# Performance work log

Hardware: AMD Instinct MI355X
Metric: run time of the kernel (lower is better)

The kernel has to match this reference:

```python
import jax, jax.numpy as jnp
import numpy as np

N = 50000
H = 8
D = 32
E = 400000
IN = 128
NEG_SLOPE = 0.2


def _gat(h, edges, W, al, ar, b):
    # DGL GATConv: fc -> per-head attention logits -> edge softmax over dst -> aggregate
    src, dst = edges[0], edges[1]
    feat = (h @ W).reshape(N, H, D)                      # [N,H,D]
    el = jnp.einsum('nhd,hd->nh', feat, al)              # [N,H]
    er = jnp.einsum('nhd,hd->nh', feat, ar)              # [N,H]
    e = jax.nn.leaky_relu(el[src] + er[dst], NEG_SLOPE)  # [E,H]
    m = jax.ops.segment_max(e, dst, num_segments=N)      # [N,H] per-dst max
    m = jnp.where(jnp.isfinite(m), m, 0.0)
    m = jax.lax.stop_gradient(m)
    ex = jnp.exp(e - m[dst])                             # [E,H]
    denom = jax.ops.segment_sum(ex, dst, num_segments=N) # [N,H]
    alpha = ex / denom[dst]                              # edge softmax
    out = jax.ops.segment_sum(feat[src] * alpha[:, :, None], dst, num_segments=N)  # [N,H,D]
    return (out + b.reshape(1, H, D)).reshape(N, H * D)


def setup_inputs() -> dict:
    key = jax.random.key(0)
    ks = jax.random.split(key, 12)
    s = 0.05
    return {
        'h': jax.random.normal(ks[0], (N, IN), jnp.float32),
        'edges0': jax.random.randint(ks[1], (2, E), 0, N, jnp.int32),
        'edges1': jax.random.randint(ks[2], (2, E), 0, N, jnp.int32),
        'fc0': jax.random.normal(ks[3], (IN, H * D), jnp.float32) * s,
        'al0': jax.random.normal(ks[4], (H, D), jnp.float32) * s,
        'ar0': jax.random.normal(ks[5], (H, D), jnp.float32) * s,
        'bias0': jnp.zeros((H * D,), jnp.float32),
        'fc1': jax.random.normal(ks[6], (IN, H * D), jnp.float32) * s,
        'al1': jax.random.normal(ks[7], (H, D), jnp.float32) * s,
        'ar1': jax.random.normal(ks[8], (H, D), jnp.float32) * s,
        'bias1': jnp.zeros((H * D,), jnp.float32),
        'sw1': jax.random.normal(ks[9], (H * D, 128), jnp.float32) * s,
        'sb1': jnp.zeros((128,), jnp.float32),
        'sw2': jax.random.normal(ks[10], (128, 1), jnp.float32) * s,
    }


def reference(h, edges0, edges1, fc0, al0, ar0, bias0, fc1, al1, ar1, bias1, sw1, sb1, sw2):
    z0 = _gat(h, edges0, fc0, al0, ar0, bias0)   # [N, H*D]
    z1 = _gat(h, edges1, fc1, al1, ar1, bias1)   # [N, H*D]
    z = jnp.stack([z0, z1], axis=1)              # [N, M=2, H*D]
    # semantic attention: MLP -> mean over nodes -> softmax over meta-paths
    w = jnp.tanh(z @ sw1 + sb1) @ sw2            # [N,M,1]
    beta = jax.nn.softmax(w.mean(axis=0), axis=0)  # [M,1]
    return (beta[None] * z).sum(axis=1)          # [N, H*D]
```

## Files before the change

kernel.cpp:

```cpp
#include <hip/hip_runtime.h>
#include <math.h>

#define NEG_SLOPE 0.2f

typedef unsigned int uint;
typedef unsigned short ushort;
typedef __bf16 bf16x8 __attribute__((ext_vector_type(8)));
typedef float f32x4 __attribute__((ext_vector_type(4)));

__device__ __forceinline__ uint bf16r(float a) {
    uint u = __float_as_uint(a);
    return (u + 0x7fffu + ((u >> 16) & 1u)) >> 16;
}
__device__ __forceinline__ uint bf16pack(float a, float b) {
    return bf16r(a) | (bf16r(b) << 16);
}
__device__ __forceinline__ float bflo(uint u) { return __uint_as_float(u << 16); }
__device__ __forceinline__ float bfhi(uint u) { return __uint_as_float(u & 0xffff0000u); }

__device__ __forceinline__ float fast_tanh(float x) {
    x = fminf(fmaxf(x, -15.f), 15.f);
    float t = __expf(2.f * x);
    return 1.f - 2.f * __builtin_amdgcn_rcpf(t + 1.f);
}

__global__ void prep_kernel(const float* __restrict__ fc0, const float* __restrict__ fc1,
                            const float* __restrict__ sw1, ushort* __restrict__ wbt,
                            ushort* __restrict__ sw1t, float* __restrict__ wsum,
                            int* __restrict__ count, int* __restrict__ cursor, int Ntot) {
    int b = blockIdx.x;
    if (b == 0 && threadIdx.x == 0) { wsum[0] = 0.f; wsum[1] = 0.f; }
    if (b < 256) {
        int idx = b * 256 + threadIdx.x;
        const float* W = (idx >> 15) ? fc1 : fc0;
        int r = idx & 32767;
        int c = r >> 7, k = r & 127;
        wbt[idx] = (ushort)bf16r(W[(size_t)k * 256 + c]);
    } else if (b < 384) {
        int idx = (b - 256) * 256 + threadIdx.x;
        int c = idx >> 8, p = idx & 255;
        int col = (p & ~63) + ((p & 3) * 16) + ((p >> 2) & 15);
        sw1t[idx] = (ushort)bf16r(sw1[(size_t)col * 128 + c]);
    } else {
        int i = (b - 384) * 256 + threadIdx.x;
        if (i < Ntot) { count[i] = 0; cursor[i] = 0; }
    }
}

__global__ void hist_kernel(const int* __restrict__ e0, const int* __restrict__ e1,
                            int* __restrict__ count, int E, int N) {
    int e = blockIdx.x * blockDim.x + threadIdx.x;
    if (e >= 2 * E) return;
    int l = (e >= E);
    int ee = e - l * E;
    const int* edges = l ? e1 : e0;
    atomicAdd(&count[edges[E + ee] + l * N], 1);
}

__global__ void scan1_kernel(const int* __restrict__ count, int* __restrict__ base,
                             int* __restrict__ bsum, int Ntot) {
    __shared__ int ws_s[4];
    int b = blockIdx.x;
    int i = b * 256 + threadIdx.x;
    int v = (i < Ntot) ? count[i] : 0;
    int lane = threadIdx.x & 63;
    int wid = threadIdx.x >> 6;
    int x = v;
#pragma unroll
    for (int s = 1; s < 64; s <<= 1) {
        int y = __shfl_up(x, s, 64);
        if (lane >= s) x += y;
    }
    if (lane == 63) ws_s[wid] = x;
    __syncthreads();
    int add = 0;
    for (int w = 0; w < wid; w++) add += ws_s[w];
    int incl = x + add;
    if (i < Ntot) base[i] = incl - v;
    if (threadIdx.x == 255) bsum[b] = incl;
}

__global__ void scan2_kernel(int* __restrict__ bsum, int nb) {
    __shared__ int ws_s[4];
    __shared__ int running_s;
    if (threadIdx.x == 0) running_s = 0;
    __syncthreads();
    int lane = threadIdx.x & 63;
    int wid = threadIdx.x >> 6;
    for (int c0 = 0; c0 < nb; c0 += 256) {
        int i = c0 + threadIdx.x;
        int v = (i < nb) ? bsum[i] : 0;
        int x = v;
#pragma unroll
        for (int s = 1; s < 64; s <<= 1) {
            int y = __shfl_up(x, s, 64);
            if (lane >= s) x += y;
        }
        if (lane == 63) ws_s[wid] = x;
        __syncthreads();
        int add = 0;
        for (int w = 0; w < wid; w++) add += ws_s[w];
        int incl = x + add;
        int run = running_s;
        if (i < nb) bsum[i] = run + incl - v;
        __syncthreads();
        if (threadIdx.x == 255) running_s = run + incl;
        __syncthreads();
    }
}

#define HKPAD 136
__global__ void __launch_bounds__(256, 4)
fc_kernel(const float* __restrict__ h, const ushort* __restrict__ wbt,
          const float* __restrict__ al0, const float* __restrict__ ar0,
          const float* __restrict__ al1, const float* __restrict__ ar1,
          ushort* __restrict__ featb, float* __restrict__ el,
          float* __restrict__ er, int N, int nb) {
    __shared__ ushort hs[64 * HKPAD];
    int b = blockIdx.x;
    int l = (b >= nb);
    int n0 = (b - l * nb) * 64;
    for (int t = threadIdx.x; t < 64 * 32; t += 256) {
        int r = t >> 5, i4 = t & 31;
        int n = n0 + r;
        float4 v = make_float4(0.f, 0.f, 0.f, 0.f);
        if (n < N) v = ((const float4*)h)[(size_t)n * 32 + i4];
        uint2 pk;
        pk.x = bf16pack(v.x, v.y);
        pk.y = bf16pack(v.z, v.w);
        *((uint2*)(hs + r * HKPAD + i4 * 4)) = pk;
    }
    __syncthreads();

    const ushort* wb = wbt + l * 32768;
    const float* al = l ? al1 : al0;
    const float* ar = l ? ar1 : ar0;
    ushort* fb = featb + (size_t)l * N * 256;
    float* elp = el + (size_t)l * N * 8;
    float* erp = er + (size_t)l * N * 8;

    int wv = threadIdx.x >> 6;
    int lane = threadIdx.x & 63;
    int lhi = lane >> 4, llo = lane & 15;

    f32x4 acc[4][4];
#pragma unroll
    for (int cb = 0; cb < 4; cb++)
#pragma unroll
        for (int rt = 0; rt < 4; rt++) acc[cb][rt] = (f32x4){0.f, 0.f, 0.f, 0.f};

#pragma unroll
    for (int ks = 0; ks < 4; ks++) {
        bf16x8 a[4];
#pragma unroll
        for (int rt = 0; rt < 4; rt++)
            a[rt] = *(const bf16x8*)(hs + (rt * 16 + llo) * HKPAD + ks * 32 + lhi * 8);
#pragma unroll
        for (int cb = 0; cb < 4; cb++) {
            bf16x8 bfrag = *(const bf16x8*)(wb + (size_t)(64 * wv + 16 * cb + llo) * 128 + ks * 32 + lhi * 8);
#pragma unroll
            for (int rt = 0; rt < 4; rt++)
                acc[cb][rt] = __builtin_amdgcn_mfma_f32_16x16x32_bf16(a[rt], bfrag, acc[cb][rt], 0, 0, 0);
        }
    }

    float alv0 = al[64 * wv + llo],      alv1 = al[64 * wv + 16 + llo];
    float alv2 = al[64 * wv + 32 + llo], alv3 = al[64 * wv + 48 + llo];
    float arv0 = ar[64 * wv + llo],      arv1 = ar[64 * wv + 16 + llo];
    float arv2 = ar[64 * wv + 32 + llo], arv3 = ar[64 * wv + 48 + llo];

#pragma unroll
    for (int rt = 0; rt < 4; rt++) {
#pragma unroll
        for (int reg = 0; reg < 4; reg++) {
            int n = n0 + rt * 16 + lhi * 4 + reg;
            bool valid = (n < N);
            uint2 pv;
            pv.x = bf16pack(acc[0][rt][reg], acc[1][rt][reg]);
            pv.y = bf16pack(acc[2][rt][reg], acc[3][rt][reg]);
            if (valid) *((uint2*)(fb + (size_t)n * 256 + 64 * wv + 4 * llo)) = pv;
            float pl0 = acc[0][rt][reg] * alv0 + acc[1][rt][reg] * alv1;
            float pl1 = acc[2][rt][reg] * alv2 + acc[3][rt][reg] * alv3;
            float pr0 = acc[0][rt][reg] * arv0 + acc[1][rt][reg] * arv1;
            float pr1 = acc[2][rt][reg] * arv2 + acc[3][rt][reg] * arv3;
#pragma unroll
            for (int s = 1; s <= 8; s <<= 1) {
                pl0 += __shfl_xor(pl0, s, 64);
                pl1 += __shfl_xor(pl1, s, 64);
                pr0 += __shfl_xor(pr0, s, 64);
                pr1 += __shfl_xor(pr1, s, 64);
            }
            if (llo == 0 && valid) {
                *((float2*)(elp + (size_t)n * 8 + 2 * wv)) = make_float2(pl0, pl1);
                *((float2*)(erp + (size_t)n * 8 + 2 * wv)) = make_float2(pr0, pr1);
            }
        }
    }
}

__global__ void scatter_kernel(const int* __restrict__ e0, const int* __restrict__ e1,
                               const float* __restrict__ el, const float* __restrict__ er,
                               const int* __restrict__ base, const int* __restrict__ bsum,
                               int* __restrict__ cursor, int* __restrict__ csr_src,
                               float* __restrict__ pedge, int E, int N) {
    int e = blockIdx.x * blockDim.x + threadIdx.x;
    if (e >= 2 * E) return;
    int l = (e >= E);
    int ee = e - l * E;
    const int* edges = l ? e1 : e0;
    int src = edges[ee];
    int dst = edges[E + ee];
    int d = dst + l * N;
    int pos = base[d] + bsum[d >> 8] + atomicAdd(&cursor[d], 1);
    csr_src[pos] = src;
    size_t so = (size_t)(l * N + src) * 2;
    size_t dofs = (size_t)(l * N + dst) * 2;
    float4 l0 = ((const float4*)el)[so];
    float4 l1 = ((const float4*)el)[so + 1];
    float4 r0 = ((const float4*)er)[dofs];
    float4 r1 = ((const float4*)er)[dofs + 1];
    float v[8] = {l0.x + r0.x, l0.y + r0.y, l0.z + r0.z, l0.w + r0.w,
                  l1.x + r1.x, l1.y + r1.y, l1.z + r1.z, l1.w + r1.w};
#pragma unroll
    for (int k = 0; k < 8; k++) {
        float t = (v[k] > 0.f) ? v[k] : NEG_SLOPE * v[k];
        v[k] = __expf(t);
    }
    ((float4*)pedge)[pos * 2]     = make_float4(v[0], v[1], v[2], v[3]);
    ((float4*)pedge)[pos * 2 + 1] = make_float4(v[4], v[5], v[6], v[7]);
}

#define AGG_STEP(qq, uu)                                        \
    d0 += (qq).x; d1 += (qq).y;                                 \
    a.x += (qq).x * bflo((uu).x); a.y += (qq).x * bfhi((uu).x); \
    a.z += (qq).y * bflo((uu).y); a.w += (qq).y * bfhi((uu).y);

__global__ void aggregate_csr_kernel(const int* __restrict__ csr_src, const float* __restrict__ pedge,
                                     const int* __restrict__ base, const int* __restrict__ bsum,
                                     const int* __restrict__ count, const ushort* __restrict__ featb,
                                     const float* __restrict__ bias0, const float* __restrict__ bias1,
                                     ushort* __restrict__ z0b, ushort* __restrict__ z1b, int N) {
    int wid = threadIdx.x >> 6;
    int lane = threadIdx.x & 63;
    int d = blockIdx.x * 4 + wid;
    if (d >= 2 * N) return;
    int l = (d >= N);
    int dst = d - l * N;
    int row0 = base[d] + bsum[d >> 8];
    int deg = count[d];
    int w = lane >> 4, llo = lane & 15;
    const float2* pe = (const float2*)(pedge + (size_t)row0 * 8);
    const int* cs = csr_src + row0;
    const uint2* fb2 = (const uint2*)(featb + (size_t)l * N * 256);

    float d0 = 0.f, d1 = 0.f;
    float4 a = make_float4(0.f, 0.f, 0.f, 0.f);
    int t = 0;
    for (; t + 8 <= deg; t += 8) {
        int s[8];
#pragma unroll
        for (int j = 0; j < 8; j++) s[j] = cs[t + j];
        float2 q[8];
#pragma unroll
        for (int j = 0; j < 8; j++) q[j] = pe[(t + j) * 4 + w];
        uint2 u[8];
#pragma unroll
        for (int j = 0; j < 8; j++) u[j] = fb2[(size_t)s[j] * 64 + lane];
#pragma unroll
        for (int j = 0; j < 8; j++) { AGG_STEP(q[j], u[j]) }
    }
    for (; t + 4 <= deg; t += 4) {
        int s[4];
#pragma unroll
        for (int j = 0; j < 4; j++) s[j] = cs[t + j];
        float2 q[4];
#pragma unroll
        for (int j = 0; j < 4; j++) q[j] = pe[(t + j) * 4 + w];
        uint2 u[4];
#pragma unroll
        for (int j = 0; j < 4; j++) u[j] = fb2[(size_t)s[j] * 64 + lane];
#pragma unroll
        for (int j = 0; j < 4; j++) { AGG_STEP(q[j], u[j]) }
    }
    for (; t < deg; t++) {
        int s0 = cs[t];
        float2 q0 = pe[t * 4 + w];
        uint2 u0 = fb2[(size_t)s0 * 64 + lane];
        AGG_STEP(q0, u0)
    }
    const float* bias = l ? bias1 : bias0;
    int c0 = 64 * w + llo;
    float b0 = bias[c0], b1 = bias[c0 + 16], b2 = bias[c0 + 32], b3 = bias[c0 + 48];
    float i0 = (d0 > 0.f) ? 1.f / d0 : 0.f;
    float i1 = (d1 > 0.f) ? 1.f / d1 : 0.f;
    uint2 o;
    o.x = bf16pack(a.x * i0 + b0, a.y * i0 + b1);
    o.y = bf16pack(a.z * i1 + b2, a.w * i1 + b3);
    ushort* zb = l ? z1b : z0b;
    ((uint2*)zb)[(size_t)dst * 64 + lane] = o;
}

#define ZROW 264
__global__ void __launch_bounds__(256, 4)
semantic_kernel(const ushort* __restrict__ z0b, const ushort* __restrict__ z1b,
                const ushort* __restrict__ sw1t, const float* __restrict__ sb1,
                const float* __restrict__ sw2, float* __restrict__ wsum, int N) {
    __shared__ ushort zs[64 * ZROW];
    __shared__ float rowp[64];
    int n0 = blockIdx.x * 32;
    if (threadIdx.x < 64) rowp[threadIdx.x] = 0.f;
    for (int t = threadIdx.x; t < 64 * 32; t += 256) {
        int row = t >> 5, i16 = t & 31;
        int r = row >> 1, mm = row & 1;
        int n = n0 + r;
        uint4 v = make_uint4(0u, 0u, 0u, 0u);
        if (n < N) v = ((const uint4*)(mm ? z1b : z0b))[(size_t)n * 32 + i16];
        *((uint4*)(zs + row * ZROW + i16 * 8)) = v;
    }
    __syncthreads();

    int wv = threadIdx.x >> 6;
    int lane = threadIdx.x & 63;
    int lhi = lane >> 4, llo = lane & 15;

    f32x4 acc[2][4];
#pragma unroll
    for (int c = 0; c < 2; c++)
#pragma unroll
        for (int rt = 0; rt < 4; rt++) acc[c][rt] = (f32x4){0.f, 0.f, 0.f, 0.f};

#pragma unroll
    for (int ks = 0; ks < 8; ks++) {
        bf16x8 b0 = *(const bf16x8*)(sw1t + (size_t)((2 * wv) * 16 + llo) * 256 + ks * 32 + lhi * 8);
        bf16x8 b1 = *(const bf16x8*)(sw1t + (size_t)((2 * wv + 1) * 16 + llo) * 256 + ks * 32 + lhi * 8);
#pragma unroll
        for (int rt = 0; rt < 4; rt++) {
            bf16x8 av = *(const bf16x8*)(zs + (rt * 16 + llo) * ZROW + ks * 32 + lhi * 8);
            acc[0][rt] = __builtin_amdgcn_mfma_f32_16x16x32_bf16(av, b0, acc[0][rt], 0, 0, 0);
            acc[1][rt] = __builtin_amdgcn_mfma_f32_16x16x32_bf16(av, b1, acc[1][rt], 0, 0, 0);
        }
    }

    float sb0 = sb1[(2 * wv) * 16 + llo],      s20 = sw2[(2 * wv) * 16 + llo];
    float sb1v = sb1[(2 * wv + 1) * 16 + llo], s21 = sw2[(2 * wv + 1) * 16 + llo];
#pragma unroll
    for (int rt = 0; rt < 4; rt++) {
        float pr[4];
#pragma unroll
        for (int reg = 0; reg < 4; reg++)
            pr[reg] = fast_tanh(acc[0][rt][reg] + sb0) * s20 + fast_tanh(acc[1][rt][reg] + sb1v) * s21;
#pragma unroll
        for (int s = 1; s <= 8; s <<= 1)
#pragma unroll
            for (int reg = 0; reg < 4; reg++) pr[reg] += __shfl_xor(pr[reg], s, 64);
        if (llo == 0) {
#pragma unroll
            for (int reg = 0; reg < 4; reg++)
                atomicAdd(&rowp[rt * 16 + lhi * 4 + reg], pr[reg]);
        }
    }
    __syncthreads();
    if (threadIdx.x < 64) {
        int node = n0 + (threadIdx.x >> 1);
        float v = (node < N) ? rowp[threadIdx.x] : 0.f;
        v += __shfl_xor(v, 2, 64);
        v += __shfl_xor(v, 4, 64);
        v += __shfl_xor(v, 8, 64);
        v += __shfl_xor(v, 16, 64);
        v += __shfl_xor(v, 32, 64);
        if (threadIdx.x < 2) atomicAdd(&wsum[threadIdx.x], v);
    }
}

__global__ void combine_kernel(float* __restrict__ out, const ushort* __restrict__ z0b,
                               const ushort* __restrict__ z1b, const float* __restrict__ wsum,
                               float invN, int N) {
    int idx = blockIdx.x * 256 + threadIdx.x;
    if (idx >= N * 64) return;
    float w0 = wsum[0] * invN, w1 = wsum[1] * invN;
    float mx = fmaxf(w0, w1);
    float e0 = __expf(w0 - mx), e1 = __expf(w1 - mx);
    float b0 = e0 / (e0 + e1), b1 = e1 / (e0 + e1);
    int n = idx >> 6, lane = idx & 63;
    int w = lane >> 4, llo = lane & 15;
    uint2 a = ((const uint2*)z0b)[idx];
    uint2 b = ((const uint2*)z1b)[idx];
    float* o = out + (size_t)n * 256 + 64 * w + llo;
    o[0]  = b0 * bflo(a.x) + b1 * bflo(b.x);
    o[16] = b0 * bfhi(a.x) + b1 * bfhi(b.x);
    o[32] = b0 * bflo(a.y) + b1 * bflo(b.y);
    o[48] = b0 * bfhi(a.y) + b1 * bfhi(b.y);
}

extern "C" void kernel_launch(void* const* d_in, const int* in_sizes, int n_in,
                              void* d_out, int out_size, void* d_ws, size_t ws_size,
                              hipStream_t stream) {
    const float* h      = (const float*)d_in[0];
    const int*   edges0 = (const int*)d_in[1];
    const int*   edges1 = (const int*)d_in[2];
    const float* fc0    = (const float*)d_in[3];
    const float* al0    = (const float*)d_in[4];
    const float* ar0    = (const float*)d_in[5];
    const float* bias0  = (const float*)d_in[6];
    const float* fc1    = (const float*)d_in[7];
    const float* al1    = (const float*)d_in[8];
    const float* ar1    = (const float*)d_in[9];
    const float* bias1  = (const float*)d_in[10];
    const float* sw1    = (const float*)d_in[11];
    const float* sb1    = (const float*)d_in[12];
    const float* sw2    = (const float*)d_in[13];

    const int N = in_sizes[0] / 128;
    const int E = in_sizes[1] / 2;
    const int Ntot = 2 * N;
    const int NB2 = (Ntot + 255) / 256;
    const int nb = (N + 63) / 64;

    char* ws = (char*)d_ws;
    ushort* featb = (ushort*)ws;
    ushort* z0b   = featb + (size_t)Ntot * 256;
    ushort* z1b   = z0b + (size_t)N * 256;
    ushort* wbt   = z1b + (size_t)N * 256;
    ushort* sw1t  = wbt + 2 * 256 * 128;
    float*  el    = (float*)(sw1t + 128 * 256);
    float*  er    = el + (size_t)Ntot * 8;
    float*  pedge = er + (size_t)Ntot * 8;
    int*    csr_src = (int*)(pedge + (size_t)E * 16);
    int*    count   = csr_src + 2 * E;
    int*    base    = count + Ntot;
    int*    cursor  = base + Ntot;
    int*    bsum    = cursor + Ntot;
    float*  wsum  = (float*)(bsum + NB2 + 2);
    float*  outp  = (float*)d_out;

    prep_kernel<<<384 + NB2, 256, 0, stream>>>(fc0, fc1, sw1, wbt, sw1t, wsum,
                                               count, cursor, Ntot);
    hist_kernel<<<(2 * E + 255) / 256, 256, 0, stream>>>(edges0, edges1, count, E, N);
    scan1_kernel<<<NB2, 256, 0, stream>>>(count, base, bsum, Ntot);
    scan2_kernel<<<1, 256, 0, stream>>>(bsum, NB2);
    fc_kernel<<<2 * nb, 256, 0, stream>>>(h, wbt, al0, ar0, al1, ar1, featb, el, er, N, nb);
    scatter_kernel<<<(2 * E + 255) / 256, 256, 0, stream>>>(edges0, edges1, el, er, base, bsum,
                                                            cursor, csr_src, pedge, E, N);
    aggregate_csr_kernel<<<(Ntot + 3) / 4, 256, 0, stream>>>(csr_src, pedge, base, bsum, count,
                                                             featb, bias0, bias1, z0b, z1b, N);
    semantic_kernel<<<(N + 31) / 32, 256, 0, stream>>>(z0b, z1b, sw1t, sb1, sw2, wsum, N);
    combine_kernel<<<(N * 64 + 255) / 256, 256, 0, stream>>>(outp, z0b, z1b, wsum,
                                                             1.0f / (float)N, N);
}
```

Measured before the change: 264.9 us.

## Split each destination row's aggregation across two wavefronts

The aggregation kernel now assigns two wavefronts per destination node, each handling half of the 256-column row with one uint (two bf16) per lane instead of a uint2. This doubles the number of wavefronts to raise parallelism and memory-level concurrency for the gather. The 8-edge unroll is removed, leaving a 4-edge unroll. In exchange, the CSR index and edge-weight loads are duplicated across both halves, and each gather becomes narrower.

```diff
diff --git a/kernel.cpp b/kernel.cpp
--- a/kernel.cpp
+++ b/kernel.cpp
@@ -230,11 +230,6 @@
     ((float4*)pedge)[pos * 2 + 1] = make_float4(v[4], v[5], v[6], v[7]);
 }
 
-#define AGG_STEP(qq, uu)                                        \
-    d0 += (qq).x; d1 += (qq).y;                                 \
-    a.x += (qq).x * bflo((uu).x); a.y += (qq).x * bfhi((uu).x); \
-    a.z += (qq).y * bflo((uu).y); a.w += (qq).y * bfhi((uu).y);
-
 __global__ void aggregate_csr_kernel(const int* __restrict__ csr_src, const float* __restrict__ pedge,
                                      const int* __restrict__ base, const int* __restrict__ bsum,
                                      const int* __restrict__ count, const ushort* __restrict__ featb,
@@ -242,62 +237,51 @@
                                      ushort* __restrict__ z0b, ushort* __restrict__ z1b, int N) {
     int wid = threadIdx.x >> 6;
     int lane = threadIdx.x & 63;
-    int d = blockIdx.x * 4 + wid;
-    if (d >= 2 * N) return;
+    int gw = blockIdx.x * 4 + wid;
+    if (gw >= 4 * N) return;
+    int d = gw >> 1, half = gw & 1;
     int l = (d >= N);
     int dst = d - l * N;
     int row0 = base[d] + bsum[d >> 8];
     int deg = count[d];
-    int w = lane >> 4, llo = lane & 15;
-    const float2* pe = (const float2*)(pedge + (size_t)row0 * 8);
+    int hh = 4 * half + ((lane >> 5) << 1) + (lane & 1);
+    int lo = half * 64 + lane;
+    int p0 = 2 * lo, p1 = p0 + 1;
+    int c0 = 64 * (p0 >> 6) + 16 * (p0 & 3) + ((p0 >> 2) & 15);
+    int c1 = 64 * (p1 >> 6) + 16 * (p1 & 3) + ((p1 >> 2) & 15);
+
     const int* cs = csr_src + row0;
-    const uint2* fb2 = (const uint2*)(featb + (size_t)l * N * 256);
-
-    float d0 = 0.f, d1 = 0.f;
-    float4 a = make_float4(0.f, 0.f, 0.f, 0.f);
+    const float* pe = pedge + row0 * 8 + hh;
+    const uint* fbu = (const uint*)featb + l * N * 128;
+
+    float dacc = 0.f, a0 = 0.f, a1 = 0.f;
     int t = 0;
-    for (; t + 8 <= deg; t += 8) {
-        int s[8];
-#pragma unroll
-        for (int j = 0; j < 8; j++) s[j] = cs[t + j];
-        float2 q[8];
-#pragma unroll
-        for (int j = 0; j < 8; j++) q[j] = pe[(t + j) * 4 + w];
-        uint2 u[8];
-#pragma unroll
-        for (int j = 0; j < 8; j++) u[j] = fb2[(size_t)s[j] * 64 + lane];
-#pragma unroll
-        for (int j = 0; j < 8; j++) { AGG_STEP(q[j], u[j]) }
-    }
     for (; t + 4 <= deg; t += 4) {
-        int s[4];
-#pragma unroll
-        for (int j = 0; j < 4; j++) s[j] = cs[t + j];
-        float2 q[4];
-#pragma unroll
-        for (int j = 0; j < 4; j++) q[j] = pe[(t + j) * 4 + w];
-        uint2 u[4];
-#pragma unroll
-        for (int j = 0; j < 4; j++) u[j] = fb2[(size_t)s[j] * 64 + lane];
-#pragma unroll
-        for (int j = 0; j < 4; j++) { AGG_STEP(q[j], u[j]) }
+        int s0 = cs[t], s1 = cs[t + 1], s2 = cs[t + 2], s3 = cs[t + 3];
+        float q0 = pe[t * 8];
+        float q1 = pe[t * 8 + 8];
+        float q2 = pe[t * 8 + 16];
+        float q3 = pe[t * 8 + 24];
+        uint u0 = fbu[s0 * 128 + lo];
+        uint u1 = fbu[s1 * 128 + lo];
+        uint u2 = fbu[s2 * 128 + lo];
+        uint u3 = fbu[s3 * 128 + lo];
+        dacc += q0; a0 += q0 * bflo(u0); a1 += q0 * bfhi(u0);
+        dacc += q1; a0 += q1 * bflo(u1); a1 += q1 * bfhi(u1);
+        dacc += q2; a0 += q2 * bflo(u2); a1 += q2 * bfhi(u2);
+        dacc += q3; a0 += q3 * bflo(u3); a1 += q3 * bfhi(u3);
     }
     for (; t < deg; t++) {
         int s0 = cs[t];
-        float2 q0 = pe[t * 4 + w];
-        uint2 u0 = fb2[(size_t)s0 * 64 + lane];
-        AGG_STEP(q0, u0)
+        float q0 = pe[t * 8];
+        uint u0 = fbu[s0 * 128 + lo];
+        dacc += q0; a0 += q0 * bflo(u0); a1 += q0 * bfhi(u0);
     }
     const float* bias = l ? bias1 : bias0;
-    int c0 = 64 * w + llo;
-    float b0 = bias[c0], b1 = bias[c0 + 16], b2 = bias[c0 + 32], b3 = bias[c0 + 48];
-    float i0 = (d0 > 0.f) ? 1.f / d0 : 0.f;
-    float i1 = (d1 > 0.f) ? 1.f / d1 : 0.f;
-    uint2 o;
-    o.x = bf16pack(a.x * i0 + b0, a.y * i0 + b1);
-    o.y = bf16pack(a.z * i1 + b2, a.w * i1 + b3);
-    ushort* zb = l ? z1b : z0b;
-    ((uint2*)zb)[(size_t)dst * 64 + lane] = o;
+    float inv = (dacc > 0.f) ? 1.f / dacc : 0.f;
+    uint o = bf16pack(a0 * inv + bias[c0], a1 * inv + bias[c1]);
+    uint* zb = (uint*)(l ? z1b : z0b);
+    zb[dst * 128 + lo] = o;
 }
 
 #define ZROW 264
@@ -441,8 +425,8 @@
     fc_kernel<<<2 * nb, 256, 0, stream>>>(h, wbt, al0, ar0, al1, ar1, featb, el, er, N, nb);
     scatter_kernel<<<(2 * E + 255) / 256, 256, 0, stream>>>(edges0, edges1, el, er, base, bsum,
                                                             cursor, csr_src, pedge, E, N);
-    aggregate_csr_kernel<<<(Ntot + 3) / 4, 256, 0, stream>>>(csr_src, pedge, base, bsum, count,
-                                                             featb, bias0, bias1, z0b, z1b, N);
+    aggregate_csr_kernel<<<N, 256, 0, stream>>>(csr_src, pedge, base, bsum, count,
+                                                featb, bias0, bias1, z0b, z1b, N);
     semantic_kernel<<<(N + 31) / 32, 256, 0, stream>>>(z0b, z1b, sw1t, sb1, sw2, wsum, N);
     combine_kernel<<<(N * 64 + 255) / 256, 256, 0, stream>>>(outp, z0b, z1b, wsum,
                                                              1.0f / (float)N, N);
```

Measured after the change: 281.2 us. 1.06x slower.
